# Performance work log

Hardware: AMD Instinct MI355X
Metric: run time of the kernel (lower is better)

The kernel has to match this reference:

```python
import math
import jax, jax.numpy as jnp
import numpy as np

C = 128; NH = 8; NL = 4; NP = 4; DFF = 512; L = 3
RH, RW = 80, 240           # Rworld_shape
H, W = RH // 2, RW // 2    # per-level spatial shape after stride-2 downsample


def setup_inputs() -> dict:
    key = jax.random.key(0)
    ks = jax.random.split(key, 25)
    def n(k, shape, s=0.02):
        return jax.random.normal(k, shape, dtype=jnp.float32) * s
    return {
        "x": jax.random.normal(ks[0], (1, NL, C, RH, RW), dtype=jnp.float32),
        "dconv_w": n(ks[1], (C, C, 3, 3)),
        "dconv_b": n(ks[2], (C,)),
        "lvl_emb": n(ks[3], (NL, C), 1.0),
        "W_off": n(ks[4], (L, NH * NL * NP * 2, C)),
        "b_off": n(ks[5], (L, NH * NL * NP * 2), 0.1),
        "W_attn": n(ks[6], (L, NH * NL * NP, C)),
        "b_attn": n(ks[7], (L, NH * NL * NP)),
        "W_val": n(ks[8], (L, C, C)),
        "b_val": n(ks[9], (L, C)),
        "W_out": n(ks[10], (L, C, C)),
        "b_out": n(ks[11], (L, C)),
        "ln1_g": jnp.ones((L, C), jnp.float32),
        "ln1_b": jnp.zeros((L, C), jnp.float32),
        "W_ff1": n(ks[12], (L, DFF, C)),
        "b_ff1": n(ks[13], (L, DFF)),
        "W_ff2": n(ks[14], (L, C, DFF)),
        "b_ff2": n(ks[15], (L, C)),
        "ln2_g": jnp.ones((L, C), jnp.float32),
        "ln2_b": jnp.zeros((L, C), jnp.float32),
        "merge_w": n(ks[16], (C, C * NL, 1, 1)),
        "merge_b": n(ks[17], (C,)),
        "uconv_w": n(ks[18], (C, C, 3, 3)),
        "uconv_b": n(ks[19], (C,)),
    }


def conv2d(x, w, b, stride=1, pad=1):
    y = jax.lax.conv_general_dilated(x, w, (stride, stride), [(pad, pad), (pad, pad)],
                                     dimension_numbers=("NCHW", "OIHW", "NCHW"))
    return y + b[None, :, None, None]


def linear(x, w, b):
    return jnp.einsum("...i,oi->...o", x, w) + b


def layer_norm(x, g, b, eps=1e-5):
    m = jnp.mean(x, -1, keepdims=True)
    v = jnp.var(x, -1, keepdims=True)
    return (x - m) * jax.lax.rsqrt(v + eps) * g + b


def sine_pos_embed(h, w, nf, temperature=10000.0):
    # matches create_pos_embedding with normalize=True, scale=2*pi
    scale = 2.0 * math.pi
    eps = 1e-6
    ye = jnp.arange(1, h + 1, dtype=jnp.float32) / (h + eps) * scale
    xe = jnp.arange(1, w + 1, dtype=jnp.float32) / (w + eps) * scale
    i = jnp.arange(nf, dtype=jnp.float32)
    dim_t = temperature ** (2.0 * jnp.floor(i / 2.0) / nf)
    def enc(e):
        p = e[:, None] / dim_t
        return jnp.stack([jnp.sin(p[:, 0::2]), jnp.cos(p[:, 1::2])], -1).reshape(e.shape[0], nf)
    py, px = enc(ye), enc(xe)
    pos = jnp.concatenate([jnp.broadcast_to(py[:, None, :], (h, w, nf)),
                           jnp.broadcast_to(px[None, :, :], (h, w, nf))], -1)
    return pos  # (h, w, 2*nf) with [pos_y, pos_x] channel order


def ms_deform_attn_core(vmaps, loc, attn):
    # vmaps: (B,NL,NH,H*W,hd); loc: (B,Lq,NH,NL,NP,2) in [0,1] (x,y); attn: (B,Lq,NH,NL,NP)
    # grid_sample(align_corners=False, padding_mode='zeros') bilinear gather
    x = loc[..., 0] * W - 0.5
    y = loc[..., 1] * H - 0.5
    x0 = jnp.floor(x)
    y0 = jnp.floor(y)
    out = jnp.zeros((loc.shape[0], loc.shape[1], NH, vmaps.shape[-1]), loc.dtype)
    for dy in (0, 1):
        for dx in (0, 1):
            xc = x0 + dx
            yc = y0 + dy
            wgt = (1.0 - jnp.abs(x - xc)) * (1.0 - jnp.abs(y - yc))
            valid = (xc >= 0) & (xc < W) & (yc >= 0) & (yc < H)
            xi = jnp.clip(xc, 0, W - 1).astype(jnp.int32)
            yi = jnp.clip(yc, 0, H - 1).astype(jnp.int32)
            idx = (yi * W + xi).transpose(0, 3, 2, 1, 4)  # (B,NL,NH,Lq,NP)
            B_, nl, nh, lq, npt = idx.shape
            g = jnp.take_along_axis(vmaps, idx.reshape(B_, nl, nh, lq * npt, 1),
                                    axis=3).reshape(B_, nl, nh, lq, npt, -1)
            wv = (wgt * jnp.where(valid, 1.0, 0.0) * attn).transpose(0, 3, 2, 1, 4)
            out = out + jnp.einsum("blhqp,blhqpd->bqhd", wv, g)
    return out.reshape(out.shape[0], out.shape[1], -1)  # (B,Lq,NH*hd)


def reference(x, dconv_w, dconv_b, lvl_emb, W_off, b_off, W_attn, b_attn, W_val, b_val,
              W_out, b_out, ln1_g, ln1_b, W_ff1, b_ff1, W_ff2, b_ff2, ln2_g, ln2_b,
              merge_w, merge_b, uconv_w, uconv_b):
    B, N, c, h0, w0 = x.shape
    xs = jax.nn.relu(conv2d(x.reshape(B * N, c, h0, w0), dconv_w, dconv_b, stride=2))
    src = xs.reshape(B, N, c, H, W).transpose(0, 1, 3, 4, 2).reshape(B, N * H * W, c)
    pos = sine_pos_embed(H, W, c // 2).reshape(1, H * W, c) + lvl_emb[:, None, :]
    pos = pos.reshape(1, N * H * W, c)
    # reference points: per-level pixel centers (valid_ratios are all ones)
    ry = (jnp.arange(H, dtype=jnp.float32) + 0.5) / H
    rx = (jnp.arange(W, dtype=jnp.float32) + 0.5) / W
    ref = jnp.stack(jnp.meshgrid(rx, ry, indexing="xy"), -1).reshape(H * W, 2)
    ref = jnp.tile(ref, (N, 1))[None]  # (1, Lq, 2)
    hd = c // NH
    norm = jnp.array([W, H], jnp.float32)
    for i in range(W_off.shape[0]):
        q = src + pos
        value = linear(src, W_val[i], b_val[i]).reshape(B, N, H * W, NH, hd)
        vmaps = value.transpose(0, 1, 3, 2, 4)  # (B,NL,NH,HW,hd)
        off = linear(q, W_off[i], b_off[i]).reshape(B, -1, NH, N, NP, 2)
        aw = jax.nn.softmax(linear(q, W_attn[i], b_attn[i]).reshape(B, -1, NH, N * NP), -1)
        aw = aw.reshape(B, -1, NH, N, NP)
        loc = ref[:, :, None, None, None, :] + off / norm
        attn_out = ms_deform_attn_core(vmaps, loc, aw)
        src = layer_norm(src + linear(attn_out, W_out[i], b_out[i]), ln1_g[i], ln1_b[i])
        ff = linear(jax.nn.relu(linear(src, W_ff1[i], b_ff1[i])), W_ff2[i], b_ff2[i])
        src = layer_norm(src + ff, ln2_g[i], ln2_b[i])
    m = src.reshape(B, N, H, W, c).transpose(0, 1, 4, 2, 3).reshape(B, N * c, H, W)
    m = jax.nn.relu(conv2d(m, merge_w, merge_b, pad=0))
    m = jax.image.resize(m, (B, c, RH, RW), method="bilinear")
    m = jax.nn.relu(conv2d(m, uconv_w, uconv_b))
    return m
```

## Files before the change

### kernel.cpp

```cpp
#include <hip/hip_runtime.h>
#include <math.h>
#include <cstddef>

#define LQ   19200
#define HH   40
#define WW   120
#define HWp  4800
#define CCh  128
#define NHd  8
#define NLv  4
#define NPt  4
#define RHs  80
#define RWs  240

typedef __attribute__((ext_vector_type(8))) short bf16x8;
typedef __attribute__((ext_vector_type(4))) float f32x4;
typedef __attribute__((ext_vector_type(8))) _Float16 h16x8;
typedef __attribute__((address_space(1))) const unsigned int GUI;
typedef __attribute__((address_space(3))) unsigned int LUI;

__device__ inline unsigned short f2bf(float f) {
    unsigned int u = __float_as_uint(f);
    u += 0x7fffu + ((u >> 16) & 1u);
    return (unsigned short)(u >> 16);
}
__device__ inline float bf2f(unsigned int lo16) { return __uint_as_float(lo16 << 16); }

template<bool BIAS_ROW, bool RELU, int OMODE>
__global__ __launch_bounds__(256) void gemm_bf16(
    const unsigned short* __restrict__ A,
    const unsigned short* __restrict__ Bw,
    const float* __restrict__ bias,
    float* __restrict__ OutF, unsigned short* __restrict__ OutB,
    int M, int N, int K)
{
    constexpr int BM = 128, BN = 64, BK = 32;
    __shared__ unsigned short As[BM * BK];
    __shared__ unsigned short Bs[BN * BK];
    const int bm = blockIdx.y * BM, bn = blockIdx.x * BN;
    const int tid = threadIdx.x;
    const int wid = tid >> 6, lane = tid & 63;
    const int wm = (wid & 1) * 64, wn = (wid >> 1) * 32;
    const int lm = lane & 15, lqd = lane >> 4;

    f32x4 acc[4][2] = {};

    const int arow = lane >> 2;
    const int akc  = (lane & 3) * 8;
    const unsigned short* aG0 = A  + (size_t)(bm + wid * 32 +      arow) * K + akc;
    const unsigned short* aG1 = A  + (size_t)(bm + wid * 32 + 16 + arow) * K + akc;
    const unsigned short* bG  = Bw + (size_t)(bn + wid * 16 +      arow) * K + akc;
    unsigned short* aL0 = As + wid * 1024 + lane * 8;
    unsigned short* aL1 = As + wid * 1024 + 512 + lane * 8;
    unsigned short* bL  = Bs + wid * 512 + lane * 8;

    for (int k0 = 0; k0 < K; k0 += BK) {
        __builtin_amdgcn_global_load_lds((GUI*)(aG0 + k0), (LUI*)aL0, 16, 0, 0);
        __builtin_amdgcn_global_load_lds((GUI*)(aG1 + k0), (LUI*)aL1, 16, 0, 0);
        __builtin_amdgcn_global_load_lds((GUI*)(bG  + k0), (LUI*)bL,  16, 0, 0);
        __syncthreads();
        bf16x8 a[4], b[2];
        #pragma unroll
        for (int i = 0; i < 4; i++)
            a[i] = *(const bf16x8*)(As + (wm + i * 16 + lm) * BK + lqd * 8);
        #pragma unroll
        for (int j = 0; j < 2; j++)
            b[j] = *(const bf16x8*)(Bs + (wn + j * 16 + lm) * BK + lqd * 8);
        #pragma unroll
        for (int i = 0; i < 4; i++)
            #pragma unroll
            for (int j = 0; j < 2; j++)
                acc[i][j] = __builtin_amdgcn_mfma_f32_16x16x32_bf16(a[i], b[j], acc[i][j], 0, 0, 0);
        __syncthreads();
    }

    #pragma unroll
    for (int i = 0; i < 4; i++) {
        int row0 = bm + wm + i * 16 + lqd * 4;
        #pragma unroll
        for (int j = 0; j < 2; j++) {
            int col = bn + wn + j * 16 + lm;
            float bc = BIAS_ROW ? 0.f : bias[col];
            #pragma unroll
            for (int r = 0; r < 4; r++) {
                int row = row0 + r;
                float v = acc[i][j][r] + (BIAS_ROW ? bias[row] : bc);
                if (RELU) v = fmaxf(v, 0.f);
                size_t o = (size_t)row * N + col;
                if (OMODE == 0) OutF[o] = v;
                else if (OMODE == 1) OutB[o] = f2bf(v);
                else { OutF[o] = v; OutB[o] = f2bf(v); }
            }
        }
    }
}

__global__ __launch_bounds__(256) void gemm_oav(
    const unsigned short* __restrict__ Aq,
    const unsigned short* __restrict__ Asrc,
    const unsigned short* __restrict__ Woa, const float* __restrict__ boa,
    const unsigned short* __restrict__ Wv,  const float* __restrict__ bv,
    _Float16* __restrict__ OutH, _Float16* __restrict__ OutH2,
    unsigned short* __restrict__ OutV)
{
    constexpr int BK = 32, K = 128;
    __shared__ unsigned short As[128 * BK];
    __shared__ unsigned short Bs[64 * BK];
    const int bx = blockIdx.x;
    const bool isv = bx >= 6;
    const unsigned short* A  = isv ? Asrc : Aq;
    const unsigned short* Bw = isv ? Wv : Woa;
    const float* bias = isv ? bv : boa;
    const int bn = isv ? (bx - 6) * 64 : bx * 64;
    const int bm = blockIdx.y * 128;
    const int tid = threadIdx.x;
    const int wid = tid >> 6, lane = tid & 63;
    const int wm = (wid & 1) * 64, wn = (wid >> 1) * 32;
    const int lm = lane & 15, lqd = lane >> 4;

    f32x4 acc[4][2] = {};

    const int arow = lane >> 2;
    const int akc  = (lane & 3) * 8;
    const unsigned short* aG0 = A  + (size_t)(bm + wid * 32 +      arow) * K + akc;
    const unsigned short* aG1 = A  + (size_t)(bm + wid * 32 + 16 + arow) * K + akc;
    const unsigned short* bG  = Bw + (size_t)(bn + wid * 16 +      arow) * K + akc;
    unsigned short* aL0 = As + wid * 1024 + lane * 8;
    unsigned short* aL1 = As + wid * 1024 + 512 + lane * 8;
    unsigned short* bL  = Bs + wid * 512 + lane * 8;

    for (int k0 = 0; k0 < K; k0 += BK) {
        __builtin_amdgcn_global_load_lds((GUI*)(aG0 + k0), (LUI*)aL0, 16, 0, 0);
        __builtin_amdgcn_global_load_lds((GUI*)(aG1 + k0), (LUI*)aL1, 16, 0, 0);
        __builtin_amdgcn_global_load_lds((GUI*)(bG  + k0), (LUI*)bL,  16, 0, 0);
        __syncthreads();
        bf16x8 a[4], b[2];
        #pragma unroll
        for (int i = 0; i < 4; i++)
            a[i] = *(const bf16x8*)(As + (wm + i * 16 + lm) * BK + lqd * 8);
        #pragma unroll
        for (int j = 0; j < 2; j++)
            b[j] = *(const bf16x8*)(Bs + (wn + j * 16 + lm) * BK + lqd * 8);
        #pragma unroll
        for (int i = 0; i < 4; i++)
            #pragma unroll
            for (int j = 0; j < 2; j++)
                acc[i][j] = __builtin_amdgcn_mfma_f32_16x16x32_bf16(a[i], b[j], acc[i][j], 0, 0, 0);
        __syncthreads();
    }

    #pragma unroll
    for (int i = 0; i < 4; i++) {
        int row0 = bm + wm + i * 16 + lqd * 4;
        #pragma unroll
        for (int j = 0; j < 2; j++) {
            int col = bn + wn + j * 16 + lm;
            float bc = bias[col];
            if (!isv) {
                if (col < 256) {
                    #pragma unroll
                    for (int r = 0; r < 4; r++)
                        OutH[(size_t)(row0 + r) * 256 + col] = (_Float16)(acc[i][j][r] + bc);
                } else {
                    #pragma unroll
                    for (int r = 0; r < 4; r++) {
                        float v = acc[i][j][r] + bc;
                        float m = v;
                        #pragma unroll
                        for (int msk = 1; msk < 16; msk <<= 1)
                            m = fmaxf(m, __shfl_xor(m, msk));
                        float e = __expf(v - m);
                        float s = e;
                        #pragma unroll
                        for (int msk = 1; msk < 16; msk <<= 1)
                            s += __shfl_xor(s, msk);
                        OutH2[(size_t)(row0 + r) * 128 + (col - 256)] = (_Float16)(e / s);
                    }
                }
            } else {
                #pragma unroll
                for (int r = 0; r < 4; r++) {
                    int row = row0 + r;
                    int plane = (row / HWp) * 8 + (col >> 4);
                    size_t o = ((size_t)plane * HWp + (row % HWp)) * 16 + (col & 15);
                    OutV[o] = f2bf(acc[i][j][r] + bc);
                }
            }
        }
    }
}

template<bool WQ, bool WMERGE>
__global__ __launch_bounds__(256) void attn_ff(
    const unsigned short* __restrict__ attnout, const float* __restrict__ srcF_in,
    const unsigned short* __restrict__ Wout, const float* __restrict__ bout,
    const float* __restrict__ g1, const float* __restrict__ c1,
    const unsigned short* __restrict__ Wff1, const float* __restrict__ bff1,
    const unsigned short* __restrict__ Wff2, const float* __restrict__ bff2,
    const float* __restrict__ g2, const float* __restrict__ c2,
    float* __restrict__ outF, unsigned short* __restrict__ outB,
    const float* __restrict__ pos, unsigned short* __restrict__ qb,
    unsigned short* __restrict__ mergeb)
{
    __shared__ unsigned short fs[32 * 136];
    __shared__ unsigned short y1s[32 * 136];
    __shared__ float red[4][2][32];
    const int bm = blockIdx.x * 32;
    const int tid = threadIdx.x;
    const int wid = tid >> 6, lane = tid & 63;
    const int lm = lane & 15, lqd = lane >> 4;
    const int wn2 = wid * 32;

    float y1r[2][2][4];
    {
        f32x4 accA[2][2] = {};
        for (int k0 = 0; k0 < 128; k0 += 32) {
            bf16x8 a[2], b[2];
            #pragma unroll
            for (int i = 0; i < 2; i++)
                a[i] = *(const bf16x8*)(attnout + (size_t)(bm + i * 16 + lm) * 128 + k0 + lqd * 8);
            #pragma unroll
            for (int j = 0; j < 2; j++)
                b[j] = *(const bf16x8*)(Wout + (size_t)(wn2 + j * 16 + lm) * 128 + k0 + lqd * 8);
            #pragma unroll
            for (int i = 0; i < 2; i++)
                #pragma unroll
                for (int j = 0; j < 2; j++)
                    accA[i][j] = __builtin_amdgcn_mfma_f32_16x16x32_bf16(a[i], b[j], accA[i][j], 0, 0, 0);
        }
        #pragma unroll
        for (int i = 0; i < 2; i++)
            #pragma unroll
            for (int j = 0; j < 2; j++) {
                int col = wn2 + j * 16 + lm;
                float bc = bout[col];
                #pragma unroll
                for (int r = 0; r < 4; r++) {
                    int row = bm + i * 16 + lqd * 4 + r;
                    y1r[i][j][r] = accA[i][j][r] + bc + srcF_in[(size_t)row * 128 + col];
                }
            }
    }
    #pragma unroll
    for (int i = 0; i < 2; i++) {
        #pragma unroll
        for (int r = 0; r < 4; r++) {
            float s = y1r[i][0][r] + y1r[i][1][r];
            float q = y1r[i][0][r] * y1r[i][0][r] + y1r[i][1][r] * y1r[i][1][r];
            #pragma unroll
            for (int msk = 1; msk < 16; msk <<= 1) {
                s += __shfl_xor(s, msk);
                q += __shfl_xor(q, msk);
            }
            if (lm == 0) {
                int rl = i * 16 + lqd * 4 + r;
                red[wid][0][rl] = s;
                red[wid][1][rl] = q;
            }
        }
    }
    __syncthreads();
    #pragma unroll
    for (int i = 0; i < 2; i++) {
        float mean[4], inv[4];
        #pragma unroll
        for (int r = 0; r < 4; r++) {
            int rl = i * 16 + lqd * 4 + r;
            float s = red[0][0][rl] + red[1][0][rl] + red[2][0][rl] + red[3][0][rl];
            float q = red[0][1][rl] + red[1][1][rl] + red[2][1][rl] + red[3][1][rl];
            float m = s * (1.0f / 128.0f);
            float v = q * (1.0f / 128.0f) - m * m;
            mean[r] = m;
            inv[r] = rsqrtf(v + 1e-5f);
        }
        #pragma unroll
        for (int j = 0; j < 2; j++) {
            int col = wn2 + j * 16 + lm;
            float gc = g1[col], bc = c1[col];
            #pragma unroll
            for (int r = 0; r < 4; r++) {
                float y = (y1r[i][j][r] - mean[r]) * inv[r] * gc + bc;
                y1r[i][j][r] = y;
                y1s[(i * 16 + lqd * 4 + r) * 136 + col] = f2bf(y);
            }
        }
    }
    __syncthreads();

    f32x4 acc2[2][2] = {};
    for (int qc = 0; qc < 4; qc++) {
        {
            f32x4 accB[2][2] = {};
            const int wn = qc * 128 + wid * 32;
            for (int k0 = 0; k0 < 128; k0 += 32) {
                bf16x8 a[2], b[2];
                #pragma unroll
                for (int i = 0; i < 2; i++)
                    a[i] = *(const bf16x8*)(y1s + (i * 16 + lm) * 136 + k0 + lqd * 8);
                #pragma unroll
                for (int j = 0; j < 2; j++)
                    b[j] = *(const bf16x8*)(Wff1 + (size_t)(wn + j * 16 + lm) * 128 + k0 + lqd * 8);
                #pragma unroll
                for (int i = 0; i < 2; i++)
                    #pragma unroll
                    for (int j = 0; j < 2; j++)
                        accB[i][j] = __builtin_amdgcn_mfma_f32_16x16x32_bf16(a[i], b[j], accB[i][j], 0, 0, 0);
            }
            #pragma unroll
            for (int i = 0; i < 2; i++) {
                #pragma unroll
                for (int j = 0; j < 2; j++) {
                    int col = wid * 32 + j * 16 + lm;
                    float bc = bff1[qc * 128 + col];
                    #pragma unroll
                    for (int r = 0; r < 4; r++) {
                        int row = i * 16 + lqd * 4 + r;
                        fs[row * 136 + col] = f2bf(fmaxf(accB[i][j][r] + bc, 0.f));
                    }
                }
            }
        }
        __syncthreads();
        for (int k0 = 0; k0 < 128; k0 += 32) {
            bf16x8 a[2], b[2];
            #pragma unroll
            for (int i = 0; i < 2; i++)
                a[i] = *(const bf16x8*)(fs + (i * 16 + lm) * 136 + k0 + lqd * 8);
            #pragma unroll
            for (int j = 0; j < 2; j++)
                b[j] = *(const bf16x8*)(Wff2 + (size_t)(wn2 + j * 16 + lm) * 512 + qc * 128 + k0 + lqd * 8);
            #pragma unroll
            for (int i = 0; i < 2; i++)
                #pragma unroll
                for (int j = 0; j < 2; j++)
                    acc2[i][j] = __builtin_amdgcn_mfma_f32_16x16x32_bf16(a[i], b[j], acc2[i][j], 0, 0, 0);
        }
        __syncthreads();
    }

    float z[2][2][4];
    #pragma unroll
    for (int i = 0; i < 2; i++) {
        #pragma unroll
        for (int j = 0; j < 2; j++) {
            int col = wn2 + j * 16 + lm;
            float bc = bff2[col];
            #pragma unroll
            for (int r = 0; r < 4; r++)
                z[i][j][r] = acc2[i][j][r] + bc + y1r[i][j][r];
        }
    }
    #pragma unroll
    for (int i = 0; i < 2; i++) {
        #pragma unroll
        for (int r = 0; r < 4; r++) {
            float s = z[i][0][r] + z[i][1][r];
            float q = z[i][0][r] * z[i][0][r] + z[i][1][r] * z[i][1][r];
            #pragma unroll
            for (int msk = 1; msk < 16; msk <<= 1) {
                s += __shfl_xor(s, msk);
                q += __shfl_xor(q, msk);
            }
            if (lm == 0) {
                int rl = i * 16 + lqd * 4 + r;
                red[wid][0][rl] = s;
                red[wid][1][rl] = q;
            }
        }
    }
    __syncthreads();

    #pragma unroll
    for (int i = 0; i < 2; i++) {
        float mean[4], inv[4];
        #pragma unroll
        for (int r = 0; r < 4; r++) {
            int rl = i * 16 + lqd * 4 + r;
            float s = red[0][0][rl] + red[1][0][rl] + red[2][0][rl] + red[3][0][rl];
            float q = red[0][1][rl] + red[1][1][rl] + red[2][1][rl] + red[3][1][rl];
            float m = s * (1.0f / 128.0f);
            float v = q * (1.0f / 128.0f) - m * m;
            mean[r] = m;
            inv[r] = rsqrtf(v + 1e-5f);
        }
        #pragma unroll
        for (int j = 0; j < 2; j++) {
            int col = wn2 + j * 16 + lm;
            float gc = g2[col], bc2 = c2[col];
            #pragma unroll
            for (int r = 0; r < 4; r++) {
                int row = bm + i * 16 + lqd * 4 + r;
                float y = (z[i][j][r] - mean[r]) * inv[r] * gc + bc2;
                if constexpr (WMERGE) {
                    int n = row / HWp, pix = row % HWp;
                    mergeb[(size_t)pix * 512 + n * 128 + col] = f2bf(y);
                } else {
                    size_t o = (size_t)row * 128 + col;
                    outF[o] = y;
                    outB[o] = f2bf(y);
                    if constexpr (WQ) qb[o] = f2bf(y + pos[o]);
                }
            }
        }
    }
}

template<int MODE>
__global__ __launch_bounds__(256) void conv3x3_gemm(
    const unsigned short* __restrict__ X,
    const unsigned short* __restrict__ Wp,
    const float* __restrict__ bias,
    float* __restrict__ OutF, unsigned short* __restrict__ OutB,
    const float* __restrict__ pos, unsigned short* __restrict__ Qb)
{
    constexpr int BM = 128, BN = 64, BK = 32;
    constexpr int SMEM = (MODE == 1) ? 33792 : 12288;
    __shared__ __align__(16) unsigned char smem[SMEM];
    unsigned short* As = (unsigned short*)smem;
    unsigned short* Bs = (unsigned short*)(smem + 8192);
    const int bm = blockIdx.y * BM, bn = blockIdx.x * BN;
    const int tid = threadIdx.x;
    const int wid = tid >> 6, lane = tid & 63;
    const int wm = (wid & 1) * 64, wn = (wid >> 1) * 32;
    const int lm = lane & 15, lqd = lane >> 4;

    f32x4 acc[4][2] = {};

    const int arow = lane >> 2;
    const int akc  = (lane & 3) * 8;
    const int r0 = bm + wid * 32 + arow;
    const int r1 = r0 + 16;
    size_t bA0, bA1;
    if (MODE == 0) {
        int n0 = r0 / HWp, rem0 = r0 % HWp, oh0 = rem0 / WW, ow0 = rem0 % WW;
        int n1 = r1 / HWp, rem1 = r1 % HWp, oh1 = rem1 / WW, ow1 = rem1 % WW;
        bA0 = ((size_t)(n0 * 82 + oh0 * 2) * 242 + ow0 * 2) * 128;
        bA1 = ((size_t)(n1 * 82 + oh1 * 2) * 242 + ow1 * 2) * 128;
    } else {
        int y0 = r0 / RWs, x0 = r0 % RWs;
        int y1 = r1 / RWs, x1 = r1 % RWs;
        bA0 = ((size_t)y0 * 242 + x0) * 128;
        bA1 = ((size_t)y1 * 242 + x1) * 128;
    }
    const unsigned short* bG = Wp + (size_t)(bn + wid * 16 + arow) * 1152 + akc;
    unsigned short* aL0 = As + wid * 1024 + lane * 8;
    unsigned short* aL1 = As + wid * 1024 + 512 + lane * 8;
    unsigned short* bL  = Bs + wid * 512 + lane * 8;

    for (int chunk = 0; chunk < 36; chunk++) {
        int tap = chunk >> 2;
        int cpart = (chunk & 3) << 5;
        int ky = tap / 3, kx = tap % 3;
        int toff = (ky * 242 + kx) * 128 + cpart + akc;
        __builtin_amdgcn_global_load_lds((GUI*)(X + bA0 + toff), (LUI*)aL0, 16, 0, 0);
        __builtin_amdgcn_global_load_lds((GUI*)(X + bA1 + toff), (LUI*)aL1, 16, 0, 0);
        __builtin_amdgcn_global_load_lds((GUI*)(bG + chunk * 32), (LUI*)bL, 16, 0, 0);
        __syncthreads();
        bf16x8 a[4], b[2];
        #pragma unroll
        for (int i = 0; i < 4; i++)
            a[i] = *(const bf16x8*)(As + (wm + i * 16 + lm) * BK + lqd * 8);
        #pragma unroll
        for (int j = 0; j < 2; j++)
            b[j] = *(const bf16x8*)(Bs + (wn + j * 16 + lm) * BK + lqd * 8);
        #pragma unroll
        for (int i = 0; i < 4; i++)
            #pragma unroll
            for (int j = 0; j < 2; j++)
                acc[i][j] = __builtin_amdgcn_mfma_f32_16x16x32_bf16(a[i], b[j], acc[i][j], 0, 0, 0);
        __syncthreads();
    }

    if (MODE == 0) {
        #pragma unroll
        for (int i = 0; i < 4; i++) {
            int row0 = bm + wm + i * 16 + lqd * 4;
            #pragma unroll
            for (int j = 0; j < 2; j++) {
                int col = bn + wn + j * 16 + lm;
                float bc = bias[col];
                #pragma unroll
                for (int r = 0; r < 4; r++) {
                    float v = fmaxf(acc[i][j][r] + bc, 0.f);
                    size_t o = (size_t)(row0 + r) * 128 + col;
                    OutF[o] = v;
                    OutB[o] = f2bf(v);
                    Qb[o] = f2bf(v + pos[o]);
                }
            }
        }
    } else {
        float* Ts = (float*)smem;
        #pragma unroll
        for (int i = 0; i < 4; i++) {
            int lr0 = wm + i * 16 + lqd * 4;
            #pragma unroll
            for (int j = 0; j < 2; j++) {
                int lc = wn + j * 16 + lm;
                float bc = bias[bn + lc];
                #pragma unroll
                for (int r = 0; r < 4; r++)
                    Ts[lc * 132 + lr0 + r] = fmaxf(acc[i][j][r] + bc, 0.f);
            }
        }
        __syncthreads();
        for (int f = tid; f < 64 * 32; f += 256) {
            int ch = f >> 5, p4 = (f & 31) << 2;
            float4 v4 = *(const float4*)(Ts + ch * 132 + p4);
            *(float4*)(OutF + (size_t)(bn + ch) * 19200 + bm + p4) = v4;
        }
    }
}

__global__ __launch_bounds__(256) void prep_all(
    const float* __restrict__ W_val, const float* __restrict__ W_out,
    const float* __restrict__ W_ff1, const float* __restrict__ W_ff2,
    const float* __restrict__ merge_w,
    const float* __restrict__ Woff, const float* __restrict__ boff,
    const float* __restrict__ Wattn, const float* __restrict__ battn,
    const float* __restrict__ dconv_w, const float* __restrict__ uconv_w,
    const float* __restrict__ lvl_emb, const float* __restrict__ x,
    unsigned short* __restrict__ wb, unsigned short* __restrict__ wcat,
    float* __restrict__ bcat, unsigned short* __restrict__ dconv_wb,
    unsigned short* __restrict__ uconv_wb, unsigned short* __restrict__ xp,
    float* __restrict__ pos)
{
    __shared__ unsigned short t[240 * 36];
    int blk = blockIdx.x;
    if (blk >= 13831) {
        int b = blk - 13831;
        int ct = b & 3;
        int tmp = b >> 2;
        int y = tmp % 80, n = tmp / 80;
        const float* xin = x + (((size_t)(n * 128 + ct * 32)) * 80 + y) * 240;
        for (int f = threadIdx.x; f < 32 * 240; f += 256) {
            int c = f / 240, xc = f % 240;
            t[xc * 36 + c] = f2bf(xin[(size_t)c * 19200 + xc]);
        }
        __syncthreads();
        unsigned short* out = xp + (((size_t)(n * 82 + y + 1)) * 242 + 1) * 128 + ct * 32;
        for (int f = threadIdx.x; f < 240 * 8; f += 256) {
            int xc = f >> 3, c4 = (f & 7) << 2;
            ushort4 v = *(const ushort4*)(t + xc * 36 + c4);
            *(ushort4*)(out + (size_t)xc * 128 + c4) = v;
        }
        return;
    }
    int idx = blk * 256 + threadIdx.x;
    if (idx < 557056) {
        const float* src; int rel;
        if      (idx <  49152) { src = W_val;   rel = idx;          }
        else if (idx <  98304) { src = W_out;   rel = idx - 49152;  }
        else if (idx < 294912) { src = W_ff1;   rel = idx - 98304;  }
        else if (idx < 491520) { src = W_ff2;   rel = idx - 294912; }
        else                   { src = merge_w; rel = idx - 491520; }
        wb[idx] = f2bf(src[rel]);
    } else if (idx < 705664) {
        int j = idx - 557056;
        if (j < 147456) {
            int layer = j / 49152, r = (j / 128) % 384, c = j & 127;
            float v = (r < 256) ? Woff[((size_t)layer * 256 + r) * 128 + c]
                                : Wattn[((size_t)layer * 128 + (r - 256)) * 128 + c];
            wcat[j] = f2bf(v);
        } else if (j < 148608) {
            int k = j - 147456;
            int layer = k / 384, r = k % 384;
            bcat[k] = (r < 256) ? boff[layer * 256 + r] : battn[layer * 128 + (r - 256)];
        }
    } else if (idx < 853120) {
        int j = idx - 705664;
        int cout = j / 1152, k = j % 1152;
        int tap = k >> 7, cin = k & 127;
        dconv_wb[j] = f2bf(dconv_w[(cout * 128 + cin) * 9 + tap]);
    } else if (idx < 1000576) {
        int j = idx - 853120;
        int cout = j / 1152, k = j % 1152;
        int tap = k >> 7, cin = k & 127;
        uconv_wb[j] = f2bf(uconv_w[(cout * 128 + cin) * 9 + tap]);
    } else if (idx < 1083008) {
        int j = idx - 1000576;
        int c4 = (j & 31) << 2;
        int tt = j >> 5;
        int p = tt % 644, n = tt / 644;
        int y, xx;
        if (p < 242)      { y = 0;       xx = p;       }
        else if (p < 484) { y = 81;      xx = p - 242; }
        else if (p < 564) { y = p - 483; xx = 0;       }
        else              { y = p - 563; xx = 241;     }
        ushort4 z = {0, 0, 0, 0};
        *(ushort4*)(xp + (((size_t)(n * 82 + y)) * 242 + xx) * 128 + c4) = z;
    } else if (idx < 3540608) {
        int j = idx - 1083008;
        int c = j & 127;
        int q = j >> 7;
        int n = q / HWp, pix = q % HWp;
        int h = pix / WW, w = pix % WW;
        int cc = (c < 64) ? c : (c - 64);
        float coord = (c < 64) ? (float)(h + 1) : (float)(w + 1);
        float denom = (c < 64) ? 40.0f : 120.0f;
        float e = coord / (denom + 1e-6f) * 6.283185307179586f;
        float expo = (float)(cc & ~1) * (1.0f / 64.0f);
        float dim_t = __expf(expo * 9.2103403719761836f);
        float p = e / dim_t;
        float v = (cc & 1) ? __cosf(p) : __sinf(p);
        pos[j] = v + lvl_emb[n * CCh + c];
    }
}

__device__ inline void fma8(float* acc, float w, uint4 v)
{
    acc[0] = fmaf(w, __uint_as_float(v.x << 16),          acc[0]);
    acc[1] = fmaf(w, __uint_as_float(v.x & 0xffff0000u),  acc[1]);
    acc[2] = fmaf(w, __uint_as_float(v.y << 16),          acc[2]);
    acc[3] = fmaf(w, __uint_as_float(v.y & 0xffff0000u),  acc[3]);
    acc[4] = fmaf(w, __uint_as_float(v.z << 16),          acc[4]);
    acc[5] = fmaf(w, __uint_as_float(v.z & 0xffff0000u),  acc[5]);
    acc[6] = fmaf(w, __uint_as_float(v.w << 16),          acc[6]);
    acc[7] = fmaf(w, __uint_as_float(v.w & 0xffff0000u),  acc[7]);
}
__device__ inline unsigned int pk2(float a, float b)
{ return (unsigned int)f2bf(a) | ((unsigned int)f2bf(b) << 16); }

__global__ __launch_bounds__(256) void deform_sample(
    const unsigned short* __restrict__ val, const _Float16* __restrict__ off,
    const _Float16* __restrict__ attn, unsigned short* __restrict__ out)
{
    int t = threadIdx.x;
    int q = blockIdx.x * 128 + (t >> 1);
    int half = t & 1;
    int h = blockIdx.y;
    int pix = q % HWp;
    int qy = pix / WW, qx = pix % WW;
    const _Float16* offp = off + (size_t)q * 256 + h * 32;
    const _Float16* ap   = attn + (size_t)q * 128 + h * 16;
    h16x8 ovv[4];
    ovv[0] = *(const h16x8*)(offp);
    ovv[1] = *(const h16x8*)(offp + 8);
    ovv[2] = *(const h16x8*)(offp + 16);
    ovv[3] = *(const h16x8*)(offp + 24);
    h16x8 avv[2];
    avv[0] = *(const h16x8*)(ap);
    avv[1] = *(const h16x8*)(ap + 8);
    const unsigned short* vh = val + half * 8;
    float acc[8] = {};
    #pragma unroll
    for (int l = 0; l < 4; l++) {
        const unsigned short* vb = vh + (size_t)(l * 8 + h) * (HWp * 16);
        #pragma unroll
        for (int p = 0; p < 4; p++) {
            float ox = (float)ovv[l][2 * p];
            float oy = (float)ovv[l][2 * p + 1];
            int ai = l * 4 + p;
            float a = (float)avv[ai >> 3][ai & 7];
            float x = (float)qx + ox;
            float y = (float)qy + oy;
            float xf = floorf(x), yf = floorf(y);
            int x0 = (int)xf, y0 = (int)yf;
            float wx1 = x - xf, wy1 = y - yf;
            float wx0 = 1.f - wx1, wy0 = 1.f - wy1;
            #pragma unroll
            for (int dy = 0; dy < 2; dy++) {
                int yc = y0 + dy;
                bool vy = (unsigned)yc < (unsigned)HH;
                int yci = min(max(yc, 0), HH - 1);
                float wyv = dy ? wy1 : wy0;
                #pragma unroll
                for (int dx = 0; dx < 2; dx++) {
                    int xc = x0 + dx;
                    bool vld = vy && ((unsigned)xc < (unsigned)WW);
                    int xci = min(max(xc, 0), WW - 1);
                    float wgt = vld ? a * wyv * (dx ? wx1 : wx0) : 0.f;
                    uint4 v = *(const uint4*)(vb + (size_t)(yci * WW + xci) * 16);
                    fma8(acc, wgt, v);
                }
            }
        }
    }
    uint4 o = { pk2(acc[0], acc[1]), pk2(acc[2], acc[3]),
                pk2(acc[4], acc[5]), pk2(acc[6], acc[7]) };
    *(uint4*)(out + (size_t)q * CCh + h * 16 + half * 8) = o;
}

__global__ void upsample_nhwc(const float* __restrict__ m, unsigned short* __restrict__ up)
{
    unsigned idx = blockIdx.x * 256u + threadIdx.x;
    if (idx >= 82u * 242u * 32u) return;
    int c4 = (idx & 31) << 2;
    int p = idx >> 5;
    int px = p % 242, py = p / 242;
    ushort4 o = {0, 0, 0, 0};
    if (py >= 1 && py <= RHs && px >= 1 && px <= RWs) {
        int y = py - 1, x = px - 1;
        float fy = (y + 0.5f) * 0.5f - 0.5f;
        float fx = (x + 0.5f) * 0.5f - 0.5f;
        float fyf = floorf(fy), fxf = floorf(fx);
        int y0 = (int)fyf, x0 = (int)fxf;
        float wy = fy - fyf, wx = fx - fxf;
        int y0c = max(y0, 0), y1c = min(y0 + 1, HH - 1);
        int x0c = max(x0, 0), x1c = min(x0 + 1, WW - 1);
        unsigned short r[4];
        #pragma unroll
        for (int cc = 0; cc < 4; cc++) {
            const float* mp = m + (size_t)(c4 + cc) * HWp;
            float v00 = mp[y0c * WW + x0c], v01 = mp[y0c * WW + x1c];
            float v10 = mp[y1c * WW + x0c], v11 = mp[y1c * WW + x1c];
            float v = (1.f - wy) * ((1.f - wx) * v00 + wx * v01)
                    + wy * ((1.f - wx) * v10 + wx * v11);
            r[cc] = f2bf(v);
        }
        o.x = r[0]; o.y = r[1]; o.z = r[2]; o.w = r[3];
    }
    *(ushort4*)(up + (size_t)p * 128 + c4) = o;
}

extern "C" void kernel_launch(void* const* d_in, const int* in_sizes, int n_in,
                              void* d_out, int out_size, void* d_ws, size_t ws_size,
                              hipStream_t stream)
{
    const float* x       = (const float*)d_in[0];
    const float* dconv_w = (const float*)d_in[1];
    const float* dconv_b = (const float*)d_in[2];
    const float* lvl_emb = (const float*)d_in[3];
    const float* W_off   = (const float*)d_in[4];
    const float* b_off   = (const float*)d_in[5];
    const float* W_attn  = (const float*)d_in[6];
    const float* b_attn  = (const float*)d_in[7];
    const float* W_val   = (const float*)d_in[8];
    const float* b_val   = (const float*)d_in[9];
    const float* W_out   = (const float*)d_in[10];
    const float* b_out   = (const float*)d_in[11];
    const float* ln1_g   = (const float*)d_in[12];
    const float* ln1_b   = (const float*)d_in[13];
    const float* W_ff1   = (const float*)d_in[14];
    const float* b_ff1   = (const float*)d_in[15];
    const float* W_ff2   = (const float*)d_in[16];
    const float* b_ff2   = (const float*)d_in[17];
    const float* ln2_g   = (const float*)d_in[18];
    const float* ln2_b   = (const float*)d_in[19];
    const float* merge_w = (const float*)d_in[20];
    const float* merge_b = (const float*)d_in[21];
    const float* uconv_w = (const float*)d_in[22];
    const float* uconv_b = (const float*)d_in[23];

    char* wsb = (char*)d_ws;
    unsigned short* xp       = (unsigned short*)(wsb);
    unsigned short* up       = (unsigned short*)(wsb + 20320256);
    float*          src      = (float*)(wsb + 25400320);
    unsigned short* srcb     = (unsigned short*)(wsb + 35230720);
    float*          pos      = (float*)(wsb + 40145920);
    unsigned short* qb       = (unsigned short*)(wsb + 49976320);
    unsigned short* valb     = (unsigned short*)(wsb + 54891520);
    _Float16*       attnh    = (_Float16*)(wsb + 59806720);
    unsigned short* attnoutb = (unsigned short*)(wsb + 69637120);
    unsigned short* wb       = (unsigned short*)(wsb + 104043520);
    unsigned short* dconv_wb = (unsigned short*)(wsb + 105452544);
    unsigned short* uconv_wb = (unsigned short*)(wsb + 105747456);
    unsigned short* wcat     = (unsigned short*)(wsb + 106042368);
    float*          bcat     = (float*)(wsb + 106337280);
    _Float16*       offh     = (_Float16*)xp;
    unsigned short* merge_in = up;
    float*          mbuf     = (float*)valb;
    float* outp = (float*)d_out;

    unsigned short* W_val_b  = wb;
    unsigned short* W_out_b  = wb + 49152;
    unsigned short* W_ff1_b  = wb + 98304;
    unsigned short* W_ff2_b  = wb + 294912;
    unsigned short* merge_wb = wb + 491520;

    prep_all<<<15111, 256, 0, stream>>>(
        W_val, W_out, W_ff1, W_ff2, merge_w, W_off, b_off, W_attn, b_attn,
        dconv_w, uconv_w, lvl_emb, x,
        wb, wcat, bcat, dconv_wb, uconv_wb, xp, pos);

    conv3x3_gemm<0><<<dim3(2, 150), 256, 0, stream>>>(
        xp, dconv_wb, dconv_b, src, srcb, pos, qb);

    for (int i = 0; i < 3; i++) {
        gemm_oav<<<dim3(8, 150), 256, 0, stream>>>(
            qb, srcb,
            wcat + (size_t)i * 49152, bcat + i * 384,
            W_val_b + (size_t)i * 16384, b_val + i * 128,
            offh, attnh, valb);
        deform_sample<<<dim3(150, 8), 256, 0, stream>>>(valb, offh, attnh, attnoutb);
        if (i < 2) {
            attn_ff<true, false><<<600, 256, 0, stream>>>(
                attnoutb, src,
                W_out_b + (size_t)i * 16384, b_out + i * 128,
                ln1_g + i * 128, ln1_b + i * 128,
                W_ff1_b + (size_t)i * 65536, b_ff1 + i * 512,
                W_ff2_b + (size_t)i * 65536, b_ff2 + i * 128,
                ln2_g + i * 128, ln2_b + i * 128,
                src, srcb, pos, qb, nullptr);
        } else {
            attn_ff<false, true><<<600, 256, 0, stream>>>(
                attnoutb, src,
                W_out_b + (size_t)i * 16384, b_out + i * 128,
                ln1_g + i * 128, ln1_b + i * 128,
                W_ff1_b + (size_t)i * 65536, b_ff1 + i * 512,
                W_ff2_b + (size_t)i * 65536, b_ff2 + i * 128,
                ln2_g + i * 128, ln2_b + i * 128,
                nullptr, nullptr, nullptr, nullptr, merge_in);
        }
    }

    gemm_bf16<true, true, 0><<<dim3(75, 1), 256, 0, stream>>>(
        merge_wb, merge_in, merge_b, mbuf, nullptr, 128, 4800, 512);

    upsample_nhwc<<<2482, 256, 0, stream>>>(mbuf, up);

    conv3x3_gemm<1><<<dim3(2, 150), 256, 0, stream>>>(
        up, uconv_wb, uconv_b, outp, nullptr, nullptr, nullptr);
}
```

Before: 478.2 us.

## Pre-swizzle FF weights into MFMA fragment order and halve conv tile height

The prep kernel now stores W_out, W_ff1 and W_ff2 in bf16 in MFMA-fragment order, so each lane in attn_ff reads its B operand as one contiguous 16-byte chunk and a wave's loads are fully coalesced. The conv3x3 GEMM tile drops from 128 to 64 rows, which doubles the grid to 300 row-blocks per column so more CUs are busy on these small convolutions. The smaller tile reuses each weight tile across fewer rows and adds more blocks and barriers.

```diff
diff --git a/kernel.cpp b/kernel.cpp
--- a/kernel.cpp
+++ b/kernel.cpp
@@ -215,13 +215,14 @@
     {
         f32x4 accA[2][2] = {};
         for (int k0 = 0; k0 < 128; k0 += 32) {
+            int kc = k0 >> 5;
             bf16x8 a[2], b[2];
             #pragma unroll
             for (int i = 0; i < 2; i++)
                 a[i] = *(const bf16x8*)(attnout + (size_t)(bm + i * 16 + lm) * 128 + k0 + lqd * 8);
             #pragma unroll
             for (int j = 0; j < 2; j++)
-                b[j] = *(const bf16x8*)(Wout + (size_t)(wn2 + j * 16 + lm) * 128 + k0 + lqd * 8);
+                b[j] = *(const bf16x8*)(Wout + ((size_t)((wid * 2 + j) * 4 + kc) * 64 + lane) * 8);
             #pragma unroll
             for (int i = 0; i < 2; i++)
                 #pragma unroll
@@ -291,15 +292,15 @@
     for (int qc = 0; qc < 4; qc++) {
         {
             f32x4 accB[2][2] = {};
-            const int wn = qc * 128 + wid * 32;
             for (int k0 = 0; k0 < 128; k0 += 32) {
+                int kc = k0 >> 5;
                 bf16x8 a[2], b[2];
                 #pragma unroll
                 for (int i = 0; i < 2; i++)
                     a[i] = *(const bf16x8*)(y1s + (i * 16 + lm) * 136 + k0 + lqd * 8);
                 #pragma unroll
                 for (int j = 0; j < 2; j++)
-                    b[j] = *(const bf16x8*)(Wff1 + (size_t)(wn + j * 16 + lm) * 128 + k0 + lqd * 8);
+                    b[j] = *(const bf16x8*)(Wff1 + ((size_t)((qc * 8 + wid * 2 + j) * 4 + kc) * 64 + lane) * 8);
                 #pragma unroll
                 for (int i = 0; i < 2; i++)
                     #pragma unroll
@@ -322,13 +323,14 @@
         }
         __syncthreads();
         for (int k0 = 0; k0 < 128; k0 += 32) {
+            int kc = qc * 4 + (k0 >> 5);
             bf16x8 a[2], b[2];
             #pragma unroll
             for (int i = 0; i < 2; i++)
                 a[i] = *(const bf16x8*)(fs + (i * 16 + lm) * 136 + k0 + lqd * 8);
             #pragma unroll
             for (int j = 0; j < 2; j++)
-                b[j] = *(const bf16x8*)(Wff2 + (size_t)(wn2 + j * 16 + lm) * 512 + qc * 128 + k0 + lqd * 8);
+                b[j] = *(const bf16x8*)(Wff2 + ((size_t)((wid * 2 + j) * 16 + kc) * 64 + lane) * 8);
             #pragma unroll
             for (int i = 0; i < 2; i++)
                 #pragma unroll
@@ -413,38 +415,32 @@
     float* __restrict__ OutF, unsigned short* __restrict__ OutB,
     const float* __restrict__ pos, unsigned short* __restrict__ Qb)
 {
-    constexpr int BM = 128, BN = 64, BK = 32;
-    constexpr int SMEM = (MODE == 1) ? 33792 : 12288;
+    constexpr int BM = 64, BN = 64, BK = 32;
+    constexpr int SMEM = (MODE == 1) ? 17408 : 8192;
     __shared__ __align__(16) unsigned char smem[SMEM];
     unsigned short* As = (unsigned short*)smem;
-    unsigned short* Bs = (unsigned short*)(smem + 8192);
+    unsigned short* Bs = (unsigned short*)(smem + 4096);
     const int bm = blockIdx.y * BM, bn = blockIdx.x * BN;
     const int tid = threadIdx.x;
     const int wid = tid >> 6, lane = tid & 63;
-    const int wm = (wid & 1) * 64, wn = (wid >> 1) * 32;
+    const int wm = (wid & 1) * 32, wn = (wid >> 1) * 32;
     const int lm = lane & 15, lqd = lane >> 4;
 
-    f32x4 acc[4][2] = {};
+    f32x4 acc[2][2] = {};
 
     const int arow = lane >> 2;
     const int akc  = (lane & 3) * 8;
-    const int r0 = bm + wid * 32 + arow;
-    const int r1 = r0 + 16;
-    size_t bA0, bA1;
+    const int r0 = bm + wid * 16 + arow;
+    size_t bA0;
     if (MODE == 0) {
         int n0 = r0 / HWp, rem0 = r0 % HWp, oh0 = rem0 / WW, ow0 = rem0 % WW;
-        int n1 = r1 / HWp, rem1 = r1 % HWp, oh1 = rem1 / WW, ow1 = rem1 % WW;
         bA0 = ((size_t)(n0 * 82 + oh0 * 2) * 242 + ow0 * 2) * 128;
-        bA1 = ((size_t)(n1 * 82 + oh1 * 2) * 242 + ow1 * 2) * 128;
     } else {
         int y0 = r0 / RWs, x0 = r0 % RWs;
-        int y1 = r1 / RWs, x1 = r1 % RWs;
         bA0 = ((size_t)y0 * 242 + x0) * 128;
-        bA1 = ((size_t)y1 * 242 + x1) * 128;
     }
     const unsigned short* bG = Wp + (size_t)(bn + wid * 16 + arow) * 1152 + akc;
-    unsigned short* aL0 = As + wid * 1024 + lane * 8;
-    unsigned short* aL1 = As + wid * 1024 + 512 + lane * 8;
+    unsigned short* aL0 = As + wid * 512 + lane * 8;
     unsigned short* bL  = Bs + wid * 512 + lane * 8;
 
     for (int chunk = 0; chunk < 36; chunk++) {
@@ -453,18 +449,17 @@
         int ky = tap / 3, kx = tap % 3;
         int toff = (ky * 242 + kx) * 128 + cpart + akc;
         __builtin_amdgcn_global_load_lds((GUI*)(X + bA0 + toff), (LUI*)aL0, 16, 0, 0);
-        __builtin_amdgcn_global_load_lds((GUI*)(X + bA1 + toff), (LUI*)aL1, 16, 0, 0);
         __builtin_amdgcn_global_load_lds((GUI*)(bG + chunk * 32), (LUI*)bL, 16, 0, 0);
         __syncthreads();
-        bf16x8 a[4], b[2];
-        #pragma unroll
-        for (int i = 0; i < 4; i++)
+        bf16x8 a[2], b[2];
+        #pragma unroll
+        for (int i = 0; i < 2; i++)
             a[i] = *(const bf16x8*)(As + (wm + i * 16 + lm) * BK + lqd * 8);
         #pragma unroll
         for (int j = 0; j < 2; j++)
             b[j] = *(const bf16x8*)(Bs + (wn + j * 16 + lm) * BK + lqd * 8);
         #pragma unroll
-        for (int i = 0; i < 4; i++)
+        for (int i = 0; i < 2; i++)
             #pragma unroll
             for (int j = 0; j < 2; j++)
                 acc[i][j] = __builtin_amdgcn_mfma_f32_16x16x32_bf16(a[i], b[j], acc[i][j], 0, 0, 0);
@@ -473,7 +468,7 @@
 
     if (MODE == 0) {
         #pragma unroll
-        for (int i = 0; i < 4; i++) {
+        for (int i = 0; i < 2; i++) {
             int row0 = bm + wm + i * 16 + lqd * 4;
             #pragma unroll
             for (int j = 0; j < 2; j++) {
@@ -492,7 +487,7 @@
     } else {
         float* Ts = (float*)smem;
         #pragma unroll
-        for (int i = 0; i < 4; i++) {
+        for (int i = 0; i < 2; i++) {
             int lr0 = wm + i * 16 + lqd * 4;
             #pragma unroll
             for (int j = 0; j < 2; j++) {
@@ -500,13 +495,13 @@
                 float bc = bias[bn + lc];
                 #pragma unroll
                 for (int r = 0; r < 4; r++)
-                    Ts[lc * 132 + lr0 + r] = fmaxf(acc[i][j][r] + bc, 0.f);
-            }
-        }
-        __syncthreads();
-        for (int f = tid; f < 64 * 32; f += 256) {
-            int ch = f >> 5, p4 = (f & 31) << 2;
-            float4 v4 = *(const float4*)(Ts + ch * 132 + p4);
+                    Ts[lc * 68 + lr0 + r] = fmaxf(acc[i][j][r] + bc, 0.f);
+            }
+        }
+        __syncthreads();
+        for (int f = tid; f < 64 * 16; f += 256) {
+            int ch = f >> 4, p4 = (f & 15) << 2;
+            float4 v4 = *(const float4*)(Ts + ch * 68 + p4);
             *(float4*)(OutF + (size_t)(bn + ch) * 19200 + bm + p4) = v4;
         }
     }
@@ -548,13 +543,29 @@
     }
     int idx = blk * 256 + threadIdx.x;
     if (idx < 557056) {
-        const float* src; int rel;
-        if      (idx <  49152) { src = W_val;   rel = idx;          }
-        else if (idx <  98304) { src = W_out;   rel = idx - 49152;  }
-        else if (idx < 294912) { src = W_ff1;   rel = idx - 98304;  }
-        else if (idx < 491520) { src = W_ff2;   rel = idx - 294912; }
-        else                   { src = merge_w; rel = idx - 491520; }
-        wb[idx] = f2bf(src[rel]);
+        if (idx < 49152) {
+            wb[idx] = f2bf(W_val[idx]);
+        } else if (idx < 98304) {
+            int rel = idx - 49152;
+            int layer = rel >> 14, within = rel & 16383;
+            int n = within >> 7, k = within & 127;
+            int frag = ((((n >> 4) * 4 + (k >> 5)) * 4 + ((k >> 3) & 3)) * 16 + (n & 15)) * 8 + (k & 7);
+            wb[49152 + (layer << 14) + frag] = f2bf(W_out[rel]);
+        } else if (idx < 294912) {
+            int rel = idx - 98304;
+            int layer = rel >> 16, within = rel & 65535;
+            int n = within >> 7, k = within & 127;
+            int frag = ((((n >> 4) * 4 + (k >> 5)) * 4 + ((k >> 3) & 3)) * 16 + (n & 15)) * 8 + (k & 7);
+            wb[98304 + (layer << 16) + frag] = f2bf(W_ff1[rel]);
+        } else if (idx < 491520) {
+            int rel = idx - 294912;
+            int layer = rel >> 16, within = rel & 65535;
+            int n = within >> 9, k = within & 511;
+            int frag = ((((n >> 4) * 16 + (k >> 5)) * 4 + ((k >> 3) & 3)) * 16 + (n & 15)) * 8 + (k & 7);
+            wb[294912 + (layer << 16) + frag] = f2bf(W_ff2[rel]);
+        } else {
+            wb[idx] = f2bf(merge_w[idx - 491520]);
+        }
     } else if (idx < 705664) {
         int j = idx - 557056;
         if (j < 147456) {
@@ -773,7 +784,7 @@
         dconv_w, uconv_w, lvl_emb, x,
         wb, wcat, bcat, dconv_wb, uconv_wb, xp, pos);
 
-    conv3x3_gemm<0><<<dim3(2, 150), 256, 0, stream>>>(
+    conv3x3_gemm<0><<<dim3(2, 300), 256, 0, stream>>>(
         xp, dconv_wb, dconv_b, src, srcb, pos, qb);
 
     for (int i = 0; i < 3; i++) {
@@ -809,6 +820,6 @@
 
     upsample_nhwc<<<2482, 256, 0, stream>>>(mbuf, up);
 
-    conv3x3_gemm<1><<<dim3(2, 150), 256, 0, stream>>>(
+    conv3x3_gemm<1><<<dim3(2, 300), 256, 0, stream>>>(
         up, uconv_wb, uconv_b, outp, nullptr, nullptr, nullptr);
 }
```

Result: faster. 440.4 us (-7.9%).
